# Performance work log

Measured on AMD Instinct MI355X. Metric: run time of the kernel, lower is better.

Reference implementation:

```python
import jax, jax.numpy as jnp
import numpy as np
from jax.ops import segment_sum

N = 100000
E = 3200000
IN_DIM = 128
HID = 64
L = 3
BN_EPS = 1e-5

def setup_inputs() -> dict:
    key = jax.random.key(0)
    ks = jax.random.split(key, 20)
    s = lambda k, *shape: jax.random.normal(k, shape, dtype=jnp.float32) * 0.05
    inp = {
        'x': jax.random.normal(ks[0], (N, IN_DIM), dtype=jnp.float32),
        'edge_index': jax.random.randint(ks[1], (2, E), 0, N, dtype=jnp.int32),
        'W_in': s(ks[2], IN_DIM, HID), 'b_in': jnp.zeros((HID,), jnp.float32),
        'W_gcn': s(ks[3], L, HID, HID), 'b_gcn': jnp.zeros((L, HID), jnp.float32),
        'bn_gamma': jnp.ones((L, HID), jnp.float32), 'bn_beta': jnp.zeros((L, HID), jnp.float32),
        'W_s1': s(ks[4], 3, HID // 2), 'b_s1': jnp.zeros((HID // 2,), jnp.float32),
        'W_s2': s(ks[5], HID // 2, HID), 'b_s2': jnp.zeros((HID,), jnp.float32),
        'W_o1': s(ks[6], 2 * HID, HID), 'b_o1': jnp.zeros((HID,), jnp.float32),
        'W_o2': s(ks[7], HID, HID // 2), 'b_o2': jnp.zeros((HID // 2,), jnp.float32),
        'W_o3': s(ks[8], HID // 2, 1), 'b_o3': jnp.zeros((1,), jnp.float32),
    }
    return inp

def _gcn_norm(row, col, n):
    # add self-loops, symmetric normalization (PyG GCNConv default)
    loop = jnp.arange(n, dtype=row.dtype)
    row_sl = jnp.concatenate([row, loop])
    col_sl = jnp.concatenate([col, loop])
    deg = segment_sum(jnp.ones_like(col_sl, jnp.float32), col_sl, num_segments=n)
    dis = jnp.where(deg > 0, jax.lax.rsqrt(jnp.maximum(deg, 1.0)), 0.0)
    norm = dis[row_sl] * dis[col_sl]
    return row_sl, col_sl, norm

def _structural(row, col, n):
    # vectorized equivalent of the O(N*E) python loops
    ones = jnp.ones(row.shape[0], jnp.float32)
    deg = segment_sum(ones, row, num_segments=n)          # out-degree over edge_index[0]
    dmax = deg.max()
    norm_deg = jnp.where(dmax > 0, deg / dmax, deg)
    infl_sum = segment_sum(deg[col], row, num_segments=n)  # sum of neighbor degrees
    infl = jnp.where(deg > 0, infl_sum / jnp.maximum(deg, 1.0), 0.0)
    imax = infl.max()
    infl = jnp.where(imax > 0, infl / imax, infl)
    clustering = jnp.zeros(n, jnp.float32)
    return jnp.stack([norm_deg, clustering, infl], axis=1)  # [N,3]

def reference(x, edge_index, W_in, b_in, W_gcn, b_gcn, bn_gamma, bn_beta,
              W_s1, b_s1, W_s2, b_s2, W_o1, b_o1, W_o2, b_o2, W_o3, b_o3):
    n = x.shape[0]
    row, col = edge_index[0], edge_index[1]
    h = x @ W_in + b_in
    row_sl, col_sl, norm = _gcn_norm(row, col, n)
    bn_scale = bn_gamma / jnp.sqrt(1.0 + BN_EPS)  # eval BN: running_mean=0, running_var=1
    for i in range(L):
        hw = h @ W_gcn[i]
        msg = hw[row_sl] * norm[:, None]              # [E+N, HID]
        h = segment_sum(msg, col_sl, num_segments=n) + b_gcn[i]
        h = h * bn_scale[i] + bn_beta[i]
        h = jax.nn.relu(h)
    sf = _structural(row, col, n)
    se = jax.nn.relu(sf @ W_s1 + b_s1) @ W_s2 + b_s2
    h = jnp.concatenate([h, se], axis=1)              # [N, 2*HID]
    h = jax.nn.relu(h @ W_o1 + b_o1)
    h = jax.nn.relu(h @ W_o2 + b_o2)
    return jax.nn.sigmoid(h @ W_o3 + b_o3)            # [N, 1]
```

## Files before the change

kernel.cpp:

```cpp
#include <hip/hip_runtime.h>
#include <hip/hip_bf16.h>
#include <hip/hip_fp16.h>

#define NBU8 65536
#define NB16 32768
#define TPBH 1024

__global__ void k_init(unsigned* __restrict__ maxima) {
    if (threadIdx.x < 2) maxima[threadIdx.x] = 0u;
}

__global__ __launch_bounds__(TPBH) void kh_hist(const int* __restrict__ keys,
                                                unsigned char* __restrict__ part,
                                                int E, int chunk, int npu) {
    __shared__ unsigned bins[NBU8 / 4];
    int b = blockIdx.x, t = threadIdx.x;
    int base = blockIdx.y * NBU8;
    int e0 = b * chunk, e1 = min(E, e0 + chunk);
    for (int j = t; j < NBU8 / 4; j += TPBH) bins[j] = 0u;
    __syncthreads();
    for (int e = e0 + t; e < e1; e += TPBH) {
        int k = keys[e] - base;
        if ((unsigned)k < NBU8) atomicAdd(&bins[k >> 2], 1u << ((k & 3) << 3));
    }
    __syncthreads();
    unsigned* dst = (unsigned*)(part + (size_t)b * npu + base);
    for (int j = t; j < NBU8 / 4; j += TPBH) dst[j] = bins[j];
}

__global__ __launch_bounds__(256) void k_scan1(const unsigned char* __restrict__ part,
                                               int nb, int npu,
                                               int* __restrict__ cnt,
                                               int* __restrict__ roff,
                                               int* __restrict__ bsum, int n) {
    __shared__ int s[256];
    int b = blockIdx.x, t = threadIdx.x;
    int i = b * 256 + t;
    int v = 0;
    if (i < n) {
        for (int k = 0; k < nb; ++k) v += part[(size_t)k * npu + i];
        cnt[i] = v;
    }
    s[t] = v;
    __syncthreads();
    for (int off = 1; off < 256; off <<= 1) {
        int x = (t >= off) ? s[t - off] : 0;
        __syncthreads();
        s[t] += x;
        __syncthreads();
    }
    if (i < n) roff[i] = s[t] - v;
    if (t == 255) bsum[b] = s[255];
}

__global__ __launch_bounds__(512) void k_scan2(int* __restrict__ bsum, int nb) {
    __shared__ int s[512];
    int t = threadIdx.x;
    int v = (t < nb) ? bsum[t] : 0;
    s[t] = v;
    __syncthreads();
    for (int off = 1; off < 512; off <<= 1) {
        int x = (t >= off) ? s[t - off] : 0;
        __syncthreads();
        s[t] += x;
        __syncthreads();
    }
    if (t < nb) bsum[t] = s[t] - v;
}

__global__ void k_scan3(int* __restrict__ roff, const int* __restrict__ bsum,
                        const int* __restrict__ cnt, float* __restrict__ dis, int n, int E) {
    int i = blockIdx.x * blockDim.x + threadIdx.x;
    if (i < n) {
        roff[i] += bsum[i >> 8];
        dis[i] = rsqrtf((float)cnt[i] + 1.0f);
    }
    if (i == 0) roff[n] = E;
}

__global__ void kh_prefix(unsigned char* __restrict__ part, int nb, int npu, int n) {
    int i = blockIdx.x * blockDim.x + threadIdx.x;
    if (i >= n) return;
    int run = 0;
    for (int g = 0; g < 8; ++g) {
        for (int b = g; b < nb; b += 8) {
            size_t idx = (size_t)b * npu + i;
            int v = part[idx];
            part[idx] = (unsigned char)run;
            run += v;
        }
    }
}

__global__ __launch_bounds__(TPBH) void kh_fill(const int* __restrict__ col,
                                                const int* __restrict__ row,
                                                const int* __restrict__ roff,
                                                const unsigned char* __restrict__ pref,
                                                int* __restrict__ esrc,
                                                int E, int chunk, int npu) {
    __shared__ unsigned curs[NBU8 / 4];
    int b = blockIdx.x, t = threadIdx.x;
    int base = blockIdx.y * NBU8;
    int e0 = b * chunk, e1 = min(E, e0 + chunk);
    for (int j = t; j < NBU8 / 4; j += TPBH) curs[j] = 0u;
    __syncthreads();
    const unsigned char* pb = pref + (size_t)b * npu;
    for (int e = e0 + t; e < e1; e += TPBH) {
        int c = col[e], r = row[e];
        int cl = c - base;
        if ((unsigned)cl < NBU8) {
            unsigned sh = (cl & 3) << 3;
            unsigned old = atomicAdd(&curs[cl >> 2], 1u << sh);
            unsigned local = (old >> sh) & 0xFFu;
            int slot = roff[c] + (int)pb[c] + (int)local;
            esrc[slot] = r;
        }
    }
}

__global__ __launch_bounds__(TPBH) void kh_histacc(const int* __restrict__ row,
                                                   const int* __restrict__ col,
                                                   const int* __restrict__ odeg_i,
                                                   unsigned short* __restrict__ part,
                                                   int E, int chunk, int npu) {
    __shared__ unsigned bins[NB16 / 2];
    int b = blockIdx.x, t = threadIdx.x;
    int base = blockIdx.y * NB16;
    int e0 = b * chunk, e1 = min(E, e0 + chunk);
    for (int j = t; j < NB16 / 2; j += TPBH) bins[j] = 0u;
    __syncthreads();
    for (int e = e0 + t; e < e1; e += TPBH) {
        int r = row[e] - base;
        if ((unsigned)r < NB16)
            atomicAdd(&bins[r >> 1], (unsigned)odeg_i[col[e]] << ((r & 1) << 4));
    }
    __syncthreads();
    unsigned* dst = (unsigned*)(part + (size_t)b * npu + base);
    for (int j = t; j < NB16 / 2; j += TPBH) dst[j] = bins[j];
}

__global__ void kh_reduce_odeg(const unsigned char* __restrict__ part,
                               float* __restrict__ odeg, int* __restrict__ odeg_i,
                               unsigned* __restrict__ maxima, int nb, int npu, int n) {
    int i = blockIdx.x * blockDim.x + threadIdx.x;
    float od = 0.f;
    if (i < n) {
        int s = 0;
        for (int b = 0; b < nb; ++b) s += part[(size_t)b * npu + i];
        od = (float)s;
        odeg[i] = od;
        odeg_i[i] = s;
    }
    for (int off = 32; off > 0; off >>= 1) od = fmaxf(od, __shfl_down(od, off));
    if ((threadIdx.x & 63) == 0) atomicMax(&maxima[0], __float_as_uint(od));
}

__global__ void kh_reduce_infl(const unsigned short* __restrict__ part,
                               const float* __restrict__ odeg,
                               float* __restrict__ infl, unsigned* __restrict__ maxima,
                               int nb, int npu, int n) {
    int i = blockIdx.x * blockDim.x + threadIdx.x;
    float fin = 0.f;
    if (i < n) {
        int s = 0;
        for (int b = 0; b < nb; ++b) s += part[(size_t)b * npu + i];
        float od = odeg[i];
        fin = (od > 0.f) ? (float)s / od : 0.f;
        infl[i] = fin;
    }
    for (int off = 32; off > 0; off >>= 1) fin = fmaxf(fin, __shfl_down(fin, off));
    if ((threadIdx.x & 63) == 0) atomicMax(&maxima[1], __float_as_uint(fin));
}

__global__ __launch_bounds__(256) void k_in_proj(const float* __restrict__ x,
                                                 const float* __restrict__ W,
                                                 const float* __restrict__ b,
                                                 float* __restrict__ h, int n) {
    __shared__ alignas(16) float Ws[128 * 64];
    __shared__ alignas(16) float xs[64 * 64];
    int t = threadIdx.x;
    int r0 = blockIdx.x * 64;
    for (int i = t; i < 128 * 64; i += 256) Ws[i] = W[i];

    int c = t & 63, rg = t >> 6;
    float acc[16];
    float bc = b[c];
#pragma unroll
    for (int i = 0; i < 16; ++i) acc[i] = bc;

    const float4* xs4 = (const float4*)xs;
    for (int half = 0; half < 2; ++half) {
        __syncthreads();
        for (int i = t; i < 64 * 16; i += 256) {
            int rr = i >> 4, k4 = i & 15;
            int r = r0 + rr;
            float4 v = (r < n) ? ((const float4*)x)[(size_t)r * 32 + half * 16 + k4]
                               : make_float4(0.f, 0.f, 0.f, 0.f);
            ((float4*)xs)[i] = v;
        }
        __syncthreads();
        for (int k4 = 0; k4 < 16; ++k4) {
            int kk = half * 64 + k4 * 4;
            float w0 = Ws[(kk + 0) * 64 + c];
            float w1 = Ws[(kk + 1) * 64 + c];
            float w2 = Ws[(kk + 2) * 64 + c];
            float w3 = Ws[(kk + 3) * 64 + c];
#pragma unroll
            for (int i = 0; i < 16; ++i) {
                float4 xv = xs4[(rg * 16 + i) * 16 + k4];
                acc[i] = fmaf(xv.x, w0, fmaf(xv.y, w1, fmaf(xv.z, w2, fmaf(xv.w, w3, acc[i]))));
            }
        }
    }
#pragma unroll
    for (int i = 0; i < 16; ++i) {
        int r = r0 + rg * 16 + i;
        if (r < n) h[(size_t)r * 64 + c] = acc[i];
    }
}

__global__ __launch_bounds__(256) void k_gcn_mm(const float* __restrict__ h,
                                                const float* __restrict__ Wg,
                                                const float* __restrict__ dis,
                                                unsigned* __restrict__ hws, int n) {
    __shared__ alignas(16) float Ws[64 * 64];
    __shared__ alignas(16) float xs[64 * 64];
    int t = threadIdx.x;
    int r0 = blockIdx.x * 64;
    for (int i = t; i < 64 * 64; i += 256) Ws[i] = Wg[i];
    for (int i = t; i < 64 * 16; i += 256) {
        int rr = i >> 4, k4 = i & 15;
        int r = r0 + rr;
        float4 v = (r < n) ? ((const float4*)h)[(size_t)r * 16 + k4]
                           : make_float4(0.f, 0.f, 0.f, 0.f);
        ((float4*)xs)[i] = v;
    }
    __syncthreads();
    int c2 = (t & 31) << 1, rg = t >> 5;
    const float4* xs4 = (const float4*)xs;
    float a0[8], a1[8];
#pragma unroll
    for (int i = 0; i < 8; ++i) { a0[i] = 0.f; a1[i] = 0.f; }
    for (int k4 = 0; k4 < 16; ++k4) {
        float wA0 = Ws[(k4 * 4 + 0) * 64 + c2],     wB0 = Ws[(k4 * 4 + 0) * 64 + c2 + 1];
        float wA1 = Ws[(k4 * 4 + 1) * 64 + c2],     wB1 = Ws[(k4 * 4 + 1) * 64 + c2 + 1];
        float wA2 = Ws[(k4 * 4 + 2) * 64 + c2],     wB2 = Ws[(k4 * 4 + 2) * 64 + c2 + 1];
        float wA3 = Ws[(k4 * 4 + 3) * 64 + c2],     wB3 = Ws[(k4 * 4 + 3) * 64 + c2 + 1];
#pragma unroll
        for (int i = 0; i < 8; ++i) {
            float4 xv = xs4[(rg * 8 + i) * 16 + k4];
            a0[i] = fmaf(xv.x, wA0, fmaf(xv.y, wA1, fmaf(xv.z, wA2, fmaf(xv.w, wA3, a0[i]))));
            a1[i] = fmaf(xv.x, wB0, fmaf(xv.y, wB1, fmaf(xv.z, wB2, fmaf(xv.w, wB3, a1[i]))));
        }
    }
#pragma unroll
    for (int i = 0; i < 8; ++i) {
        int r = r0 + rg * 8 + i;
        if (r < n) {
            float d = dis[r];
            __half2 hv = __floats2half2_rn(a0[i] * d, a1[i] * d);
            hws[(size_t)r * 32 + (t & 31)] = *(unsigned*)&hv;
        }
    }
}

__global__ __launch_bounds__(256) void k_gather(const int* __restrict__ roff,
                                                const int* __restrict__ esrc,
                                                const uint2* __restrict__ hws,
                                                const float* __restrict__ dis,
                                                const float* __restrict__ bg,
                                                const float* __restrict__ gamma,
                                                const float* __restrict__ beta,
                                                float* __restrict__ h, int n) {
    int t = threadIdx.x;
    int node = blockIdx.x * 16 + (t >> 4);
    int fl = t & 15;
    if (node >= n) return;

    int beg = roff[node], end = roff[node + 1];
    float acc0 = 0.f, acc1 = 0.f, acc2 = 0.f, acc3 = 0.f;
    union { unsigned u; __half2 h2; } cv;
#define ACC(a) { cv.u = (a).x; float2 f = __half22float2(cv.h2); acc0 += f.x; acc1 += f.y; \
                 cv.u = (a).y; f = __half22float2(cv.h2);        acc2 += f.x; acc3 += f.y; }
    {
        uint2 a = hws[(size_t)node * 16 + fl];
        ACC(a)
    }
    int e = beg;
    for (; e + 4 <= end; e += 4) {
        int r0 = esrc[e], r1 = esrc[e + 1], r2 = esrc[e + 2], r3 = esrc[e + 3];
        uint2 a = hws[(size_t)r0 * 16 + fl];
        uint2 b = hws[(size_t)r1 * 16 + fl];
        uint2 c = hws[(size_t)r2 * 16 + fl];
        uint2 d = hws[(size_t)r3 * 16 + fl];
        ACC(a) ACC(b) ACC(c) ACC(d)
    }
    for (; e < end; ++e) {
        uint2 a = hws[(size_t)esrc[e] * 16 + fl];
        ACC(a)
    }
#undef ACC
    float d = dis[node];
    float inv = rsqrtf(1.0f + 1e-5f);
    float4 g4 = ((const float4*)gamma)[fl];
    float4 b4 = ((const float4*)beta)[fl];
    float4 bg4 = ((const float4*)bg)[fl];
    float4 o;
    o.x = fmaxf(fmaf(acc0 * d + bg4.x, g4.x * inv, b4.x), 0.0f);
    o.y = fmaxf(fmaf(acc1 * d + bg4.y, g4.y * inv, b4.y), 0.0f);
    o.z = fmaxf(fmaf(acc2 * d + bg4.z, g4.z * inv, b4.z), 0.0f);
    o.w = fmaxf(fmaf(acc3 * d + bg4.w, g4.w * inv, b4.w), 0.0f);
    ((float4*)h)[(size_t)node * 16 + fl] = o;
}

__global__ __launch_bounds__(256) void k_final(const float* __restrict__ h,
                                               const float* __restrict__ odeg,
                                               const float* __restrict__ infl,
                                               const unsigned* __restrict__ maxima,
                                               const float* __restrict__ Ws1, const float* __restrict__ bs1,
                                               const float* __restrict__ Ws2, const float* __restrict__ bs2,
                                               const float* __restrict__ Wo1, const float* __restrict__ bo1,
                                               const float* __restrict__ Wo2, const float* __restrict__ bo2,
                                               const float* __restrict__ Wo3, const float* __restrict__ bo3,
                                               float* __restrict__ out, int n) {
    __shared__ alignas(16) float sWs1[96], sbs1[32], sWs2T[64 * 32], sbs2[64];
    __shared__ alignas(16) float sWo1[128 * 64], sbo1[64], sWo2[64 * 32], sbo2[32], sWo3[32];
    int t = threadIdx.x;
    for (int i = t; i < 96; i += 256) sWs1[i] = Ws1[i];
    for (int i = t; i < 2048; i += 256) {
        int j = i >> 6, k = i & 63;
        sWs2T[k * 32 + j] = Ws2[i];
    }
    for (int i = t; i < 8192; i += 256) sWo1[i] = Wo1[i];
    for (int i = t; i < 2048; i += 256) sWo2[i] = Wo2[i];
    if (t < 32) { sbs1[t] = bs1[t]; sbo2[t] = bo2[t]; sWo3[t] = Wo3[t]; }
    if (t < 64) { sbs2[t] = bs2[t]; sbo1[t] = bo1[t]; }
    __syncthreads();

    int i = blockIdx.x * 256 + t;
    if (i >= n) return;

    float dmax = __uint_as_float(maxima[0]);
    float imax = __uint_as_float(maxima[1]);
    float od = odeg[i];
    float sf0 = (dmax > 0.0f) ? od / dmax : od;
    float fin = infl[i];
    float sf2 = (imax > 0.0f) ? fin / imax : fin;

    float hid[32];
#pragma unroll
    for (int j = 0; j < 32; ++j)
        hid[j] = fmaxf(fmaf(sf0, sWs1[j], fmaf(sf2, sWs1[64 + j], sbs1[j])), 0.0f);

    float o1[64];
    const float4* sbo1_4 = (const float4*)sbo1;
#pragma unroll
    for (int c4 = 0; c4 < 16; ++c4) {
        float4 v = sbo1_4[c4];
        o1[c4 * 4] = v.x; o1[c4 * 4 + 1] = v.y; o1[c4 * 4 + 2] = v.z; o1[c4 * 4 + 3] = v.w;
    }

    const float4* sWo1_4 = (const float4*)sWo1;
    const float4* hrow = (const float4*)(h + (size_t)i * 64);
    for (int k4 = 0; k4 < 16; ++k4) {
        float4 hv = hrow[k4];
        float hv_[4] = {hv.x, hv.y, hv.z, hv.w};
#pragma unroll
        for (int j = 0; j < 4; ++j) {
            float hk = hv_[j];
            int k = k4 * 4 + j;
#pragma unroll
            for (int c4 = 0; c4 < 16; ++c4) {
                float4 w = sWo1_4[k * 16 + c4];
                o1[c4 * 4]     = fmaf(hk, w.x, o1[c4 * 4]);
                o1[c4 * 4 + 1] = fmaf(hk, w.y, o1[c4 * 4 + 1]);
                o1[c4 * 4 + 2] = fmaf(hk, w.z, o1[c4 * 4 + 2]);
                o1[c4 * 4 + 3] = fmaf(hk, w.w, o1[c4 * 4 + 3]);
            }
        }
    }
    const float4* sWs2T_4 = (const float4*)sWs2T;
    for (int k = 0; k < 64; ++k) {
        float sek = sbs2[k];
#pragma unroll
        for (int j4 = 0; j4 < 8; ++j4) {
            float4 w = sWs2T_4[k * 8 + j4];
            sek = fmaf(hid[j4 * 4], w.x, fmaf(hid[j4 * 4 + 1], w.y,
                  fmaf(hid[j4 * 4 + 2], w.z, fmaf(hid[j4 * 4 + 3], w.w, sek))));
        }
#pragma unroll
        for (int c4 = 0; c4 < 16; ++c4) {
            float4 w = sWo1_4[(64 + k) * 16 + c4];
            o1[c4 * 4]     = fmaf(sek, w.x, o1[c4 * 4]);
            o1[c4 * 4 + 1] = fmaf(sek, w.y, o1[c4 * 4 + 1]);
            o1[c4 * 4 + 2] = fmaf(sek, w.z, o1[c4 * 4 + 2]);
            o1[c4 * 4 + 3] = fmaf(sek, w.w, o1[c4 * 4 + 3]);
        }
    }

    float o2[32];
    const float4* sbo2_4 = (const float4*)sbo2;
#pragma unroll
    for (int c4 = 0; c4 < 8; ++c4) {
        float4 v = sbo2_4[c4];
        o2[c4 * 4] = v.x; o2[c4 * 4 + 1] = v.y; o2[c4 * 4 + 2] = v.z; o2[c4 * 4 + 3] = v.w;
    }
    const float4* sWo2_4 = (const float4*)sWo2;
#pragma unroll
    for (int c = 0; c < 64; ++c) {
        float v = fmaxf(o1[c], 0.0f);
#pragma unroll
        for (int c4 = 0; c4 < 8; ++c4) {
            float4 w = sWo2_4[c * 8 + c4];
            o2[c4 * 4]     = fmaf(v, w.x, o2[c4 * 4]);
            o2[c4 * 4 + 1] = fmaf(v, w.y, o2[c4 * 4 + 1]);
            o2[c4 * 4 + 2] = fmaf(v, w.z, o2[c4 * 4 + 2]);
            o2[c4 * 4 + 3] = fmaf(v, w.w, o2[c4 * 4 + 3]);
        }
    }

    float o3 = bo3[0];
#pragma unroll
    for (int c2 = 0; c2 < 32; ++c2)
        o3 = fmaf(fmaxf(o2[c2], 0.0f), sWo3[c2], o3);

    out[i] = 1.0f / (1.0f + __expf(-o3));
}

extern "C" void kernel_launch(void* const* d_in, const int* in_sizes, int n_in,
                              void* d_out, int out_size, void* d_ws, size_t ws_size,
                              hipStream_t stream) {
    const float* x     = (const float*)d_in[0];
    const int*   ei    = (const int*)d_in[1];
    const float* W_in  = (const float*)d_in[2];
    const float* b_in  = (const float*)d_in[3];
    const float* W_gcn = (const float*)d_in[4];
    const float* b_gcn = (const float*)d_in[5];
    const float* gamma = (const float*)d_in[6];
    const float* beta  = (const float*)d_in[7];
    const float* Ws1   = (const float*)d_in[8];
    const float* bs1   = (const float*)d_in[9];
    const float* Ws2   = (const float*)d_in[10];
    const float* bs2   = (const float*)d_in[11];
    const float* Wo1   = (const float*)d_in[12];
    const float* bo1   = (const float*)d_in[13];
    const float* Wo2   = (const float*)d_in[14];
    const float* bo2   = (const float*)d_in[15];
    const float* Wo3   = (const float*)d_in[16];
    const float* bo3   = (const float*)d_in[17];
    float* out = (float*)d_out;

    int n = in_sizes[0] / 128;
    int E = in_sizes[1] / 2;
    const int* row = ei;
    const int* col = ei + E;

    int npass8  = (n + NBU8 - 1) / NBU8;
    int npass16 = (n + NB16 - 1) / NB16;
    size_t NPU8  = (size_t)npass8 * NBU8;
    size_t NPU16 = (size_t)npass16 * NB16;

    auto al = [](size_t v) { return (v + 255) & ~(size_t)255; };
    size_t fixed = al((NPU8 + 256) * 4)
                 + al(NPU8 * 4)
                 + al(1024 * 4)
                 + 3 * al(NPU8 * 4)
                 + al(NPU8 * 4)
                 + al(256)
                 + al((size_t)E * 4)
                 + al((size_t)n * 64 * 4)
                 + al((size_t)n * 64 * 2);
    int NB = 128;
    auto partBytes = [&](int nb) {
        size_t a = (size_t)nb * NPU8, b2 = (size_t)nb * NPU16 * 2;
        return a > b2 ? a : b2;
    };
    while (NB > 32 && fixed + partBytes(NB) > ws_size) NB >>= 1;
    int chunk = (E + NB - 1) / NB;

    char* p = (char*)d_ws;
    unsigned char*  part8  = (unsigned char*)p;
    unsigned short* part16 = (unsigned short*)p;
    p += al(partBytes(NB));
    int* roff = (int*)p;        p += al((NPU8 + 256) * 4);
    int* cnt  = (int*)p;        p += al(NPU8 * 4);
    int* bsum = (int*)p;        p += al(1024 * 4);
    float* dis  = (float*)p;    p += al(NPU8 * 4);
    float* odeg = (float*)p;    p += al(NPU8 * 4);
    float* infl = (float*)p;    p += al(NPU8 * 4);
    int* odeg_i = (int*)p;      p += al(NPU8 * 4);
    unsigned* maxima = (unsigned*)p; p += al(256);
    int* esrc = (int*)p;        p += al((size_t)E * 4);
    float* h   = (float*)p;     p += al((size_t)n * 64 * 4);
    unsigned* hws = (unsigned*)p;

    int gn = (n + 255) / 256;

    k_init<<<1, 64, 0, stream>>>(maxima);

    kh_hist<<<dim3(NB, npass8), TPBH, 0, stream>>>(col, part8, E, chunk, (int)NPU8);
    k_scan1<<<gn, 256, 0, stream>>>(part8, NB, (int)NPU8, cnt, roff, bsum, n);
    k_scan2<<<1, 512, 0, stream>>>(bsum, gn);
    k_scan3<<<gn, 256, 0, stream>>>(roff, bsum, cnt, dis, n, E);
    kh_prefix<<<gn, 256, 0, stream>>>(part8, NB, (int)NPU8, n);
    kh_fill<<<dim3(NB, npass8), TPBH, 0, stream>>>(col, row, roff, part8, esrc, E, chunk, (int)NPU8);

    kh_hist<<<dim3(NB, npass8), TPBH, 0, stream>>>(row, part8, E, chunk, (int)NPU8);
    kh_reduce_odeg<<<gn, 256, 0, stream>>>(part8, odeg, odeg_i, maxima, NB, (int)NPU8, n);
    kh_histacc<<<dim3(NB, npass16), TPBH, 0, stream>>>(row, col, odeg_i, part16, E, chunk, (int)NPU16);
    kh_reduce_infl<<<gn, 256, 0, stream>>>(part16, odeg, infl, maxima, NB, (int)NPU16, n);

    k_in_proj<<<(n + 63) / 64, 256, 0, stream>>>(x, W_in, b_in, h, n);

    for (int l = 0; l < 3; ++l) {
        k_gcn_mm<<<(n + 63) / 64, 256, 0, stream>>>(h, W_gcn + (size_t)l * 64 * 64, dis, hws, n);
        k_gather<<<(n + 15) / 16, 256, 0, stream>>>(roff, esrc, (const uint2*)hws, dis,
                                                    b_gcn + l * 64, gamma + l * 64, beta + l * 64,
                                                    h, n);
    }

    k_final<<<gn, 256, 0, stream>>>(h, odeg, infl, maxima,
                                    Ws1, bs1, Ws2, bs2, Wo1, bo1, Wo2, bo2, Wo3, bo3,
                                    out, n);
}
```

Measured before the change: 799.7 us.

## Fuse input projection with first GCN matmul, widen gather loads, merge small kernels

Folds maxima initialization into kh_hist and k_scan3 into kh_prefix, removing two launches. The input projection now also applies the first GCN weight and the dis scaling, writing fp16 hws directly and skipping the fp32 h round trip plus one gcn_mm launch. The gather uses 8 lanes per node with 16-byte loads instead of 16 lanes with 8-byte loads. It doubles the histogram block count while halving it for histacc, which increases the in_proj shared-memory footprint and per-block register pressure.

```diff
diff --git a/kernel.cpp b/kernel.cpp
--- a/kernel.cpp
+++ b/kernel.cpp
@@ -6,15 +6,13 @@
 #define NB16 32768
 #define TPBH 1024
 
-__global__ void k_init(unsigned* __restrict__ maxima) {
-    if (threadIdx.x < 2) maxima[threadIdx.x] = 0u;
-}
-
 __global__ __launch_bounds__(TPBH) void kh_hist(const int* __restrict__ keys,
                                                 unsigned char* __restrict__ part,
+                                                unsigned* __restrict__ maxima,
                                                 int E, int chunk, int npu) {
     __shared__ unsigned bins[NBU8 / 4];
     int b = blockIdx.x, t = threadIdx.x;
+    if (b == 0 && blockIdx.y == 0 && t < 2) maxima[t] = 0u;
     int base = blockIdx.y * NBU8;
     int e0 = b * chunk, e1 = min(E, e0 + chunk);
     for (int j = t; j < NBU8 / 4; j += TPBH) bins[j] = 0u;
@@ -68,19 +66,14 @@
     if (t < nb) bsum[t] = s[t] - v;
 }
 
-__global__ void k_scan3(int* __restrict__ roff, const int* __restrict__ bsum,
-                        const int* __restrict__ cnt, float* __restrict__ dis, int n, int E) {
+__global__ void kh_prefix(unsigned char* __restrict__ part, int nb, int npu, int n,
+                          int* __restrict__ roff, const int* __restrict__ bsum,
+                          const int* __restrict__ cnt, float* __restrict__ dis, int E) {
     int i = blockIdx.x * blockDim.x + threadIdx.x;
-    if (i < n) {
-        roff[i] += bsum[i >> 8];
-        dis[i] = rsqrtf((float)cnt[i] + 1.0f);
-    }
     if (i == 0) roff[n] = E;
-}
-
-__global__ void kh_prefix(unsigned char* __restrict__ part, int nb, int npu, int n) {
-    int i = blockIdx.x * blockDim.x + threadIdx.x;
     if (i >= n) return;
+    roff[i] += bsum[i >> 8];
+    dis[i] = rsqrtf((float)cnt[i] + 1.0f);
     int run = 0;
     for (int g = 0; g < 8; ++g) {
         for (int b = g; b < nb; b += 8) {
@@ -175,12 +168,16 @@
 __global__ __launch_bounds__(256) void k_in_proj(const float* __restrict__ x,
                                                  const float* __restrict__ W,
                                                  const float* __restrict__ b,
-                                                 float* __restrict__ h, int n) {
+                                                 const float* __restrict__ Wg0,
+                                                 const float* __restrict__ dis,
+                                                 __half* __restrict__ hws, int n) {
     __shared__ alignas(16) float Ws[128 * 64];
     __shared__ alignas(16) float xs[64 * 64];
+    __shared__ alignas(16) float W2[64 * 64];
     int t = threadIdx.x;
     int r0 = blockIdx.x * 64;
     for (int i = t; i < 128 * 64; i += 256) Ws[i] = W[i];
+    for (int i = t; i < 64 * 64; i += 256) W2[i] = Wg0[i];
 
     int c = t & 63, rg = t >> 6;
     float acc[16];
@@ -212,10 +209,24 @@
             }
         }
     }
-#pragma unroll
+    __syncthreads();
+#pragma unroll
+    for (int i = 0; i < 16; ++i) xs[(rg * 16 + i) * 64 + c] = acc[i];
+    __syncthreads();
+#pragma unroll 2
     for (int i = 0; i < 16; ++i) {
         int r = r0 + rg * 16 + i;
-        if (r < n) h[(size_t)r * 64 + c] = acc[i];
+        if (r >= n) break;
+        float s = 0.f;
+#pragma unroll
+        for (int k4 = 0; k4 < 16; ++k4) {
+            float4 hv = xs4[(rg * 16 + i) * 16 + k4];
+            s = fmaf(hv.x, W2[(k4 * 4 + 0) * 64 + c],
+                fmaf(hv.y, W2[(k4 * 4 + 1) * 64 + c],
+                fmaf(hv.z, W2[(k4 * 4 + 2) * 64 + c],
+                fmaf(hv.w, W2[(k4 * 4 + 3) * 64 + c], s))));
+        }
+        hws[(size_t)r * 64 + c] = __float2half(s * dis[r]);
     }
 }
 
@@ -266,51 +277,60 @@
 
 __global__ __launch_bounds__(256) void k_gather(const int* __restrict__ roff,
                                                 const int* __restrict__ esrc,
-                                                const uint2* __restrict__ hws,
+                                                const uint4* __restrict__ hws,
                                                 const float* __restrict__ dis,
                                                 const float* __restrict__ bg,
                                                 const float* __restrict__ gamma,
                                                 const float* __restrict__ beta,
                                                 float* __restrict__ h, int n) {
     int t = threadIdx.x;
-    int node = blockIdx.x * 16 + (t >> 4);
-    int fl = t & 15;
+    int node = blockIdx.x * 32 + (t >> 3);
+    int ln = t & 7;
     if (node >= n) return;
 
     int beg = roff[node], end = roff[node + 1];
-    float acc0 = 0.f, acc1 = 0.f, acc2 = 0.f, acc3 = 0.f;
+    float a[8];
+#pragma unroll
+    for (int j = 0; j < 8; ++j) a[j] = 0.f;
     union { unsigned u; __half2 h2; } cv;
-#define ACC(a) { cv.u = (a).x; float2 f = __half22float2(cv.h2); acc0 += f.x; acc1 += f.y; \
-                 cv.u = (a).y; f = __half22float2(cv.h2);        acc2 += f.x; acc3 += f.y; }
+#define ACC(v) { cv.u = (v).x; float2 f_ = __half22float2(cv.h2); a[0] += f_.x; a[1] += f_.y; \
+                 cv.u = (v).y; f_ = __half22float2(cv.h2);        a[2] += f_.x; a[3] += f_.y; \
+                 cv.u = (v).z; f_ = __half22float2(cv.h2);        a[4] += f_.x; a[5] += f_.y; \
+                 cv.u = (v).w; f_ = __half22float2(cv.h2);        a[6] += f_.x; a[7] += f_.y; }
     {
-        uint2 a = hws[(size_t)node * 16 + fl];
-        ACC(a)
+        uint4 v = hws[(size_t)node * 8 + ln];
+        ACC(v)
     }
     int e = beg;
     for (; e + 4 <= end; e += 4) {
         int r0 = esrc[e], r1 = esrc[e + 1], r2 = esrc[e + 2], r3 = esrc[e + 3];
-        uint2 a = hws[(size_t)r0 * 16 + fl];
-        uint2 b = hws[(size_t)r1 * 16 + fl];
-        uint2 c = hws[(size_t)r2 * 16 + fl];
-        uint2 d = hws[(size_t)r3 * 16 + fl];
-        ACC(a) ACC(b) ACC(c) ACC(d)
+        uint4 v0 = hws[(size_t)r0 * 8 + ln];
+        uint4 v1 = hws[(size_t)r1 * 8 + ln];
+        uint4 v2 = hws[(size_t)r2 * 8 + ln];
+        uint4 v3 = hws[(size_t)r3 * 8 + ln];
+        ACC(v0) ACC(v1) ACC(v2) ACC(v3)
     }
     for (; e < end; ++e) {
-        uint2 a = hws[(size_t)esrc[e] * 16 + fl];
-        ACC(a)
+        uint4 v = hws[(size_t)esrc[e] * 8 + ln];
+        ACC(v)
     }
 #undef ACC
     float d = dis[node];
     float inv = rsqrtf(1.0f + 1e-5f);
-    float4 g4 = ((const float4*)gamma)[fl];
-    float4 b4 = ((const float4*)beta)[fl];
-    float4 bg4 = ((const float4*)bg)[fl];
-    float4 o;
-    o.x = fmaxf(fmaf(acc0 * d + bg4.x, g4.x * inv, b4.x), 0.0f);
-    o.y = fmaxf(fmaf(acc1 * d + bg4.y, g4.y * inv, b4.y), 0.0f);
-    o.z = fmaxf(fmaf(acc2 * d + bg4.z, g4.z * inv, b4.z), 0.0f);
-    o.w = fmaxf(fmaf(acc3 * d + bg4.w, g4.w * inv, b4.w), 0.0f);
-    ((float4*)h)[(size_t)node * 16 + fl] = o;
+    float4 g0 = ((const float4*)gamma)[ln * 2], g1 = ((const float4*)gamma)[ln * 2 + 1];
+    float4 b0 = ((const float4*)beta)[ln * 2],  b1 = ((const float4*)beta)[ln * 2 + 1];
+    float4 q0 = ((const float4*)bg)[ln * 2],    q1 = ((const float4*)bg)[ln * 2 + 1];
+    float4 o0, o1;
+    o0.x = fmaxf(fmaf(a[0] * d + q0.x, g0.x * inv, b0.x), 0.0f);
+    o0.y = fmaxf(fmaf(a[1] * d + q0.y, g0.y * inv, b0.y), 0.0f);
+    o0.z = fmaxf(fmaf(a[2] * d + q0.z, g0.z * inv, b0.z), 0.0f);
+    o0.w = fmaxf(fmaf(a[3] * d + q0.w, g0.w * inv, b0.w), 0.0f);
+    o1.x = fmaxf(fmaf(a[4] * d + q1.x, g1.x * inv, b1.x), 0.0f);
+    o1.y = fmaxf(fmaf(a[5] * d + q1.y, g1.y * inv, b1.y), 0.0f);
+    o1.z = fmaxf(fmaf(a[6] * d + q1.z, g1.z * inv, b1.z), 0.0f);
+    o1.w = fmaxf(fmaf(a[7] * d + q1.w, g1.w * inv, b1.w), 0.0f);
+    ((float4*)h)[(size_t)node * 16 + ln * 2]     = o0;
+    ((float4*)h)[(size_t)node * 16 + ln * 2 + 1] = o1;
 }
 
 __global__ __launch_bounds__(256) void k_final(const float* __restrict__ h,
@@ -469,14 +489,17 @@
                  + al(256)
                  + al((size_t)E * 4)
                  + al((size_t)n * 64 * 4)
-                 + al((size_t)n * 64 * 2);
-    int NB = 128;
+                 + 2 * al((size_t)n * 64 * 2);
+    int NB = 256;
     auto partBytes = [&](int nb) {
-        size_t a = (size_t)nb * NPU8, b2 = (size_t)nb * NPU16 * 2;
+        size_t a = (size_t)nb * NPU8;
+        size_t b2 = (size_t)(nb / 2) * NPU16 * 2;
         return a > b2 ? a : b2;
     };
     while (NB > 32 && fixed + partBytes(NB) > ws_size) NB >>= 1;
-    int chunk = (E + NB - 1) / NB;
+    int NBa = NB / 2;
+    int chunk  = (E + NB - 1) / NB;
+    int chunkA = (E + NBa - 1) / NBa;
 
     char* p = (char*)d_ws;
     unsigned char*  part8  = (unsigned char*)p;
@@ -492,32 +515,35 @@
     unsigned* maxima = (unsigned*)p; p += al(256);
     int* esrc = (int*)p;        p += al((size_t)E * 4);
     float* h   = (float*)p;     p += al((size_t)n * 64 * 4);
-    unsigned* hws = (unsigned*)p;
+    __half* hwsA = (__half*)p;  p += al((size_t)n * 64 * 2);
+    __half* hwsB = (__half*)p;
 
     int gn = (n + 255) / 256;
 
-    k_init<<<1, 64, 0, stream>>>(maxima);
-
-    kh_hist<<<dim3(NB, npass8), TPBH, 0, stream>>>(col, part8, E, chunk, (int)NPU8);
+    kh_hist<<<dim3(NB, npass8), TPBH, 0, stream>>>(col, part8, maxima, E, chunk, (int)NPU8);
     k_scan1<<<gn, 256, 0, stream>>>(part8, NB, (int)NPU8, cnt, roff, bsum, n);
     k_scan2<<<1, 512, 0, stream>>>(bsum, gn);
-    k_scan3<<<gn, 256, 0, stream>>>(roff, bsum, cnt, dis, n, E);
-    kh_prefix<<<gn, 256, 0, stream>>>(part8, NB, (int)NPU8, n);
+    kh_prefix<<<gn, 256, 0, stream>>>(part8, NB, (int)NPU8, n, roff, bsum, cnt, dis, E);
     kh_fill<<<dim3(NB, npass8), TPBH, 0, stream>>>(col, row, roff, part8, esrc, E, chunk, (int)NPU8);
 
-    kh_hist<<<dim3(NB, npass8), TPBH, 0, stream>>>(row, part8, E, chunk, (int)NPU8);
+    kh_hist<<<dim3(NB, npass8), TPBH, 0, stream>>>(row, part8, maxima, E, chunk, (int)NPU8);
     kh_reduce_odeg<<<gn, 256, 0, stream>>>(part8, odeg, odeg_i, maxima, NB, (int)NPU8, n);
-    kh_histacc<<<dim3(NB, npass16), TPBH, 0, stream>>>(row, col, odeg_i, part16, E, chunk, (int)NPU16);
-    kh_reduce_infl<<<gn, 256, 0, stream>>>(part16, odeg, infl, maxima, NB, (int)NPU16, n);
-
-    k_in_proj<<<(n + 63) / 64, 256, 0, stream>>>(x, W_in, b_in, h, n);
-
-    for (int l = 0; l < 3; ++l) {
-        k_gcn_mm<<<(n + 63) / 64, 256, 0, stream>>>(h, W_gcn + (size_t)l * 64 * 64, dis, hws, n);
-        k_gather<<<(n + 15) / 16, 256, 0, stream>>>(roff, esrc, (const uint2*)hws, dis,
-                                                    b_gcn + l * 64, gamma + l * 64, beta + l * 64,
-                                                    h, n);
-    }
+    kh_histacc<<<dim3(NBa, npass16), TPBH, 0, stream>>>(row, col, odeg_i, part16, E, chunkA, (int)NPU16);
+    kh_reduce_infl<<<gn, 256, 0, stream>>>(part16, odeg, infl, maxima, NBa, (int)NPU16, n);
+
+    k_in_proj<<<(n + 63) / 64, 256, 0, stream>>>(x, W_in, b_in, W_gcn, dis, hwsA, n);
+
+    int gg = (n + 31) / 32;
+    k_gather<<<gg, 256, 0, stream>>>(roff, esrc, (const uint4*)hwsA, dis,
+                                     b_gcn + 0 * 64, gamma + 0 * 64, beta + 0 * 64, h, n);
+    k_gcn_mm<<<(n + 63) / 64, 256, 0, stream>>>(h, W_gcn + (size_t)1 * 64 * 64, dis,
+                                                (unsigned*)hwsB, n);
+    k_gather<<<gg, 256, 0, stream>>>(roff, esrc, (const uint4*)hwsB, dis,
+                                     b_gcn + 1 * 64, gamma + 1 * 64, beta + 1 * 64, h, n);
+    k_gcn_mm<<<(n + 63) / 64, 256, 0, stream>>>(h, W_gcn + (size_t)2 * 64 * 64, dis,
+                                                (unsigned*)hwsA, n);
+    k_gather<<<gg, 256, 0, stream>>>(roff, esrc, (const uint4*)hwsA, dis,
+                                     b_gcn + 2 * 64, gamma + 2 * 64, beta + 2 * 64, h, n);
 
     k_final<<<gn, 256, 0, stream>>>(h, odeg, infl, maxima,
                                     Ws1, bs1, Ws2, bs2, Wo1, bo1, Wo2, bo2, Wo3, bo3,
```

Result: slower. 863.8 us (+8.0%).
